# Kernel tuning notes

Hardware: AMD Instinct MI355X
Metric: run time of the kernel (lower is better)

## Reference

```python
import jax, jax.numpy as jnp
import numpy as np
import math

HIDDEN = 768
N_HEADS = 12
HEAD = HIDDEN // N_HEADS


def setup_inputs() -> dict:
    key = jax.random.key(0)
    k1, k2, k3, k4, k5 = jax.random.split(key, 5)
    x = jax.random.normal(k1, (2, 2048, HIDDEN), dtype=jnp.float32)
    s = 1.0 / math.sqrt(HIDDEN)
    W_qkv = jax.random.uniform(k2, (HIDDEN, 3 * HIDDEN), minval=-s, maxval=s, dtype=jnp.float32)
    b_qkv = jax.random.uniform(k3, (3 * HIDDEN,), minval=-s, maxval=s, dtype=jnp.float32)
    W_out = jax.random.uniform(k4, (HIDDEN, HIDDEN), minval=-s, maxval=s, dtype=jnp.float32)
    b_out = jax.random.uniform(k5, (HIDDEN,), minval=-s, maxval=s, dtype=jnp.float32)
    return {"x": x, "W_qkv": W_qkv, "b_qkv": b_qkv, "W_out": W_out, "b_out": b_out}


def reference(x, W_qkv, b_qkv, W_out, b_out):
    b, n, _ = x.shape
    qkv = x @ W_qkv + b_qkv                      # [b, n, 3H]
    q, k, v = jnp.split(qkv, 3, axis=-1)
    def heads(t):
        return t.reshape(b, n, N_HEADS, HEAD).transpose(0, 2, 1, 3)  # b h n l
    q, k, v = heads(q), heads(k), heads(v)
    scores = jnp.einsum('bhql,bhkl->bhqk', q, k) / math.sqrt(HEAD)
    mask = jnp.arange(n)[:, None] < jnp.arange(n)[None, :]  # True above diagonal
    scores = jnp.where(mask, jnp.float32(-10000.0), scores)
    attn = jax.nn.softmax(scores, axis=-1)
    out = jnp.einsum('bhqk,bhkl->bhql', attn, v)
    out = out.transpose(0, 2, 1, 3).reshape(b, n, HIDDEN)
    return out @ W_out + b_out
```

## Files before the change

kernel.cpp:

```cpp
#include <hip/hip_runtime.h>

typedef __attribute__((ext_vector_type(8))) short short8;
typedef __attribute__((ext_vector_type(4))) short short4v;
typedef __attribute__((ext_vector_type(4))) float floatx4;
typedef __attribute__((ext_vector_type(16))) float floatx16;

#define HIDDEN 768
#define NH 12
#define HD 64
#define SEQ 2048
#define BATCH 2
#define BHN (BATCH*NH)
#define MTOT (BATCH*SEQ)
#define NQKV (3*HIDDEN)
#define QSCALE 0.1803368801111204f

__device__ __forceinline__ short f2bf(float f) {
  union { float f; unsigned u; } v; v.f = f;
  unsigned r = v.u + 0x7FFFu + ((v.u >> 16) & 1u);
  return (short)(r >> 16);
}
__device__ __forceinline__ unsigned bfrne(float f) {
  unsigned u = __float_as_uint(f);
  return u + 0x7FFFu + ((u >> 16) & 1u);
}
__device__ __forceinline__ unsigned pk2(float a, float b) {
  return __builtin_amdgcn_perm(bfrne(b), bfrne(a), 0x07060302u);
}
__device__ __forceinline__ float bf2f(short s) {
  return __uint_as_float(((unsigned)(unsigned short)s) << 16);
}
__device__ __forceinline__ floatx4 mfma_bf16(short8 a, short8 b, floatx4 c) {
  return __builtin_amdgcn_mfma_f32_16x16x32_bf16(a, b, c, 0, 0, 0);
}
__device__ __forceinline__ floatx16 mfma32(short8 a, short8 b, floatx16 c) {
  return __builtin_amdgcn_mfma_f32_32x32x16_bf16(a, b, c, 0, 0, 0);
}
__device__ __forceinline__ short8 ld8(const short* p) {
  return *reinterpret_cast<const short8*>(p);
}
__device__ __forceinline__ void glds16(const short* g, short* l) {
  __builtin_amdgcn_global_load_lds(
      (const __attribute__((address_space(1))) void*)g,
      (__attribute__((address_space(3))) void*)l, 16, 0, 0);
}

__global__ __launch_bounds__(256) void prep(const float* __restrict__ X,
                                            const float* __restrict__ Wqkv,
                                            const float* __restrict__ Wout,
                                            short* __restrict__ Xb,
                                            short* __restrict__ WqkvT,
                                            short* __restrict__ WoutT) {
  __shared__ short t[64][72];
  int bx = blockIdx.x;
  if (bx < 1536) {
    int i = (bx * 256 + threadIdx.x) * 8;
    const float4* s = reinterpret_cast<const float4*>(X + i);
    float4 v0 = s[0], v1 = s[1];
    short8 o;
    o[0] = f2bf(v0.x); o[1] = f2bf(v0.y); o[2] = f2bf(v0.z); o[3] = f2bf(v0.w);
    o[4] = f2bf(v1.x); o[5] = f2bf(v1.y); o[6] = f2bf(v1.z); o[7] = f2bf(v1.w);
    *reinterpret_cast<short8*>(Xb + i) = o;
    return;
  }
  int tt = bx - 1536;
  int bxx = tt % 48, by = tt / 48;
  const float* W; short* WT; int N; int nb;
  if (bxx < 36) { W = Wqkv; WT = WqkvT; N = NQKV;   nb = bxx * 64; }
  else          { W = Wout; WT = WoutT; N = HIDDEN; nb = (bxx - 36) * 64; }
  int kb = by * 64;
  int tid = threadIdx.x;
  {
    int k  = tid >> 2;
    int n0 = (tid & 3) << 4;
    const float4* src = reinterpret_cast<const float4*>(W + (size_t)(kb + k) * N + nb + n0);
    #pragma unroll
    for (int c = 0; c < 4; ++c) {
      float4 v = src[c];
      t[n0 + c*4 + 0][k] = f2bf(v.x);
      t[n0 + c*4 + 1][k] = f2bf(v.y);
      t[n0 + c*4 + 2][k] = f2bf(v.z);
      t[n0 + c*4 + 3][k] = f2bf(v.w);
    }
  }
  __syncthreads();
  {
    int n  = tid >> 2;
    int k0 = (tid & 3) << 4;
    const short8* row = reinterpret_cast<const short8*>(&t[n][k0]);
    short8* dst = reinterpret_cast<short8*>(WT + (size_t)(nb + n) * HIDDEN + kb + k0);
    dst[0] = row[0];
    dst[1] = row[1];
  }
}

__global__ __launch_bounds__(256) void gemm_qkv(const short* __restrict__ Xb,
                                                const short* __restrict__ WT,
                                                const float* __restrict__ bias,
                                                short* __restrict__ Qb,
                                                short* __restrict__ Kb,
                                                short* __restrict__ VTb) {
  __shared__ short As[128 * 32];
  __shared__ short Bs[128 * 32];
  int m0 = blockIdx.x * 128, n0 = blockIdx.y * 128;
  int tid = threadIdx.x;
  int lane = tid & 63, wv = tid >> 6;
  int wm = (wv >> 1) << 6, wn = (wv & 1) << 6;
  int quad = lane >> 4, l16 = lane & 15;

  int srow = lane >> 2;
  int schunk = (lane & 3) ^ ((lane >> 3) & 3);
  const short* ag0 = Xb + (size_t)(m0 + wv * 32 + srow) * HIDDEN + schunk * 8;
  const short* ag1 = ag0 + 16 * HIDDEN;
  const short* bg0 = WT + (size_t)(n0 + wv * 32 + srow) * HIDDEN + schunk * 8;
  const short* bg1 = bg0 + 16 * HIDDEN;
  short* lA0 = As + wv * 1024;
  short* lB0 = Bs + wv * 1024;

  int sw = ((l16 >> 1) & 3);
  int aoff = (wm + l16) * 32 + ((quad ^ sw) << 3);
  int boff = (wn + l16) * 32 + ((quad ^ sw) << 3);

  floatx4 acc[4][4] = {};
  for (int kk = 0; kk < HIDDEN; kk += 32) {
    __syncthreads();
    glds16(ag0, lA0);
    glds16(ag1, lA0 + 512);
    glds16(bg0, lB0);
    glds16(bg1, lB0 + 512);
    ag0 += 32; ag1 += 32; bg0 += 32; bg1 += 32;
    __syncthreads();
    short8 af[4], bfr[4];
    #pragma unroll
    for (int i = 0; i < 4; ++i)
      af[i] = *reinterpret_cast<const short8*>(&As[aoff + i * 512]);
    #pragma unroll
    for (int j = 0; j < 4; ++j)
      bfr[j] = *reinterpret_cast<const short8*>(&Bs[boff + j * 512]);
    #pragma unroll
    for (int i = 0; i < 4; ++i)
      #pragma unroll
      for (int j = 0; j < 4; ++j)
        acc[i][j] = mfma_bf16(af[i], bfr[j], acc[i][j]);
  }
  int colbase = n0 + wn;
  int part = colbase / HIDDEN;
  #pragma unroll
  for (int j = 0; j < 4; ++j) {
    int col = colbase + j * 16 + l16;
    float bs = bias[col];
    int rem = col - part * HIDDEN;
    int h = rem >> 6, d = rem & 63;
    #pragma unroll
    for (int i = 0; i < 4; ++i) {
      #pragma unroll
      for (int r = 0; r < 4; ++r) {
        int row = m0 + wm + i * 16 + quad * 4 + r;
        float v = acc[i][j][r] + bs;
        int bb = row >> 11, s = row & 2047;
        int bh = bb * NH + h;
        if (part == 0) {
          Qb[((size_t)bh * SEQ + s) * HD + d] = f2bf(v * QSCALE);
        } else if (part == 1) {
          Kb[((size_t)bh * SEQ + s) * HD + d] = f2bf(v);
        } else {
          VTb[((size_t)bh * HD + d) * SEQ + s] = f2bf(v);
        }
      }
    }
  }
}

__global__ __launch_bounds__(256, 4) void attn_partial(const short* __restrict__ Qb,
                                                       const short* __restrict__ Kb,
                                                       const short* __restrict__ VTb,
                                                       short* __restrict__ PO,
                                                       float* __restrict__ PM,
                                                       float* __restrict__ PL) {
  __shared__ __align__(16) char lds[32768];
  int blk = blockIdx.x;
  int cls = blk & 7;
  int j   = blk >> 3;
  int headsel = j / 40;
  int bh  = cls + 8 * headsel;
  int cidx = 39 - (j - headsel * 40);
  int qt, c;
  if (cidx < 4)       { qt = cidx;                  c = 0; }
  else if (cidx < 12) { qt = 4 + ((cidx - 4) >> 1); c = (cidx - 4) & 1; }
  else if (cidx < 24) { int t = cidx - 12; int q3 = t / 3; qt = 8 + q3; c = t - 3 * q3; }
  else                { int t = cidx - 24; qt = 12 + (t >> 2); c = t & 3; }
  int g = qt >> 2, p = qt & 3;
  int idx = bh * 40 + (g + 1) * (2 * g + p) + c;

  int nt  = 2 * qt + 2;
  int kt0 = c * 8;
  int kt1 = min(nt, kt0 + 8);
  int qb0 = qt * 128;

  int tid = threadIdx.x;
  int lane = tid & 63, wv = tid >> 6;
  int l31 = lane & 31, h = lane >> 5, x = lane & 7;
  const short* Qp = Qb + (size_t)bh * SEQ * HD;
  const short* Kp = Kb + (size_t)bh * SEQ * HD;
  const short* Vp = VTb + (size_t)bh * HD * SEQ;

  int qs  = qb0 + wv * 32 + l31;
  int qlo = qb0 + wv * 32;
  int qhi = qlo + 31;

  short8 bq[4];
  #pragma unroll
  for (int dc = 0; dc < 4; ++dc)
    bq[dc] = ld8(Qp + qs * HD + dc * 16 + h * 8);

  int lr = lane >> 3;
  int cgc = (lane & 7) ^ lr;
  const short* kgl = Kp + (size_t)(kt0 * 64 + wv * 16 + lr) * HD + cgc * 8;
  const short* vgl = Vp + (size_t)(wv * 16 + lr) * SEQ + kt0 * 64 + cgc * 8;
  int wofs = wv * 2048;

  int rbase[4];
  #pragma unroll
  for (int kc = 0; kc < 4; ++kc)
    rbase[kc] = (l31 << 7) | ((((kc << 1) | h) ^ x) << 4);

  glds16(kgl,            (short*)(lds + wofs));
  glds16(kgl + 8 * HD,   (short*)(lds + wofs + 1024));
  glds16(vgl,            (short*)(lds + 16384 + wofs));
  glds16(vgl + 8 * SEQ,  (short*)(lds + 16384 + wofs + 1024));
  __syncthreads();

  floatx16 o0 = {}, o1 = {};
  float m_run = -1e30f, l_run = 0.f;

  for (int kt = kt0; kt < kt1; ++kt) {
    int cur = (kt - kt0) & 1;
    int curK = cur * 8192, curV = 16384 + cur * 8192;
    int kb = kt * 64;

    if (kt + 1 < kt1) {
      kgl += 64 * HD; vgl += 64;
      int nK = (cur ^ 1) * 8192, nV = 16384 + (cur ^ 1) * 8192;
      glds16(kgl,           (short*)(lds + nK + wofs));
      glds16(kgl + 8 * HD,  (short*)(lds + nK + wofs + 1024));
      glds16(vgl,           (short*)(lds + nV + wofs));
      glds16(vgl + 8 * SEQ, (short*)(lds + nV + wofs + 1024));
    }

    if (kb <= qhi) {
      floatx16 s0 = {}, s1 = {};
      #pragma unroll
      for (int kc = 0; kc < 4; ++kc) {
        short8 ka0 = *reinterpret_cast<const short8*>(lds + curK + rbase[kc]);
        short8 ka1 = *reinterpret_cast<const short8*>(lds + curK + 4096 + rbase[kc]);
        s0 = mfma32(ka0, bq[kc], s0);
        s1 = mfma32(ka1, bq[kc], s1);
      }
      if (kb + 63 > qlo) {
        #pragma unroll
        for (int r = 0; r < 16; ++r) {
          int kvr = kb + (r & 3) + 8 * (r >> 2) + 4 * h;
          s0[r] = (kvr > qs) ? -1e30f : s0[r];
          s1[r] = (kvr + 32 > qs) ? -1e30f : s1[r];
        }
      }
      float mloc = m_run;
      #pragma unroll
      for (int r = 0; r < 16; ++r) { mloc = fmaxf(mloc, s0[r]); mloc = fmaxf(mloc, s1[r]); }
      mloc = fmaxf(mloc, __shfl_xor(mloc, 32));
      float m_new = mloc;
      float alpha = __builtin_amdgcn_exp2f(m_run - m_new);
      float sloc = 0.f;
      #pragma unroll
      for (int r = 0; r < 16; ++r) {
        s0[r] = __builtin_amdgcn_exp2f(s0[r] - m_new); sloc += s0[r];
        s1[r] = __builtin_amdgcn_exp2f(s1[r] - m_new); sloc += s1[r];
      }
      sloc += __shfl_xor(sloc, 32);
      l_run = l_run * alpha + sloc;
      m_run = m_new;
      o0 *= alpha; o1 *= alpha;
      short8 pb[4];
      #pragma unroll
      for (int kvc = 0; kvc < 4; ++kvc) {
        int base = (kvc & 1) * 8;
        const floatx16& P = (kvc < 2) ? s0 : s1;
        unsigned e0 = pk2(P[base + 0], P[base + 1]);
        unsigned e1 = pk2(P[base + 2], P[base + 3]);
        unsigned f0 = pk2(P[base + 4], P[base + 5]);
        unsigned f1 = pk2(P[base + 6], P[base + 7]);
        unsigned k_0 = h ? f0 : e0, k_1 = h ? f1 : e1;
        unsigned s_0 = h ? e0 : f0, s_1 = h ? e1 : f1;
        unsigned r_0 = __shfl_xor((int)s_0, 32);
        unsigned r_1 = __shfl_xor((int)s_1, 32);
        union { unsigned u[4]; short8 v; } pbu;
        pbu.u[0] = h ? r_0 : k_0;
        pbu.u[1] = h ? r_1 : k_1;
        pbu.u[2] = h ? k_0 : r_0;
        pbu.u[3] = h ? k_1 : r_1;
        pb[kvc] = pbu.v;
      }
      #pragma unroll
      for (int kvc = 0; kvc < 4; ++kvc) {
        short8 va0 = *reinterpret_cast<const short8*>(lds + curV + rbase[kvc]);
        short8 va1 = *reinterpret_cast<const short8*>(lds + curV + 4096 + rbase[kvc]);
        o0 = mfma32(va0, pb[kvc], o0);
        o1 = mfma32(va1, pb[kvc], o1);
      }
    }
    __syncthreads();
  }

  int qloc = wv * 32 + l31;
  size_t pobase = (size_t)idx * 8192 + qloc * 64;
  #pragma unroll
  for (int dt = 0; dt < 2; ++dt) {
    #pragma unroll
    for (int cc = 0; cc < 4; ++cc) {
      int d = dt * 32 + 8 * cc + 4 * h;
      short4v w;
      #pragma unroll
      for (int r = 0; r < 4; ++r)
        w[r] = f2bf(dt ? o1[4 * cc + r] : o0[4 * cc + r]);
      *reinterpret_cast<short4v*>(PO + pobase + d) = w;
    }
  }
  if (h == 0) {
    PM[idx * 128 + qloc] = m_run;
    PL[idx * 128 + qloc] = l_run;
  }
}

__global__ __launch_bounds__(256) void attn_merge(const short* __restrict__ PO,
                                                  const float* __restrict__ PM,
                                                  const float* __restrict__ PL,
                                                  short* __restrict__ AO) {
  int blk = blockIdx.x;
  int bh = blk >> 4, qt = blk & 15;
  int g = qt >> 2, p = qt & 3;
  int base = bh * 40 + (g + 1) * (2 * g + p);
  int nc = g + 1;
  int tid = threadIdx.x;
  int q = tid >> 1, dh = (tid & 1) << 5;
  float mv[4];
  float M = -1e30f;
  for (int c = 0; c < nc; ++c) {
    mv[c] = PM[(base + c) * 128 + q];
    M = fmaxf(M, mv[c]);
  }
  float wsum = 0.f;
  float acc[32] = {};
  for (int c = 0; c < nc; ++c) {
    float w = __builtin_amdgcn_exp2f(mv[c] - M);
    wsum += PL[(base + c) * 128 + q] * w;
    const short8* po = reinterpret_cast<const short8*>(PO + (size_t)(base + c) * 8192 + q * 64 + dh);
    #pragma unroll
    for (int k = 0; k < 4; ++k) {
      short8 v = po[k];
      #pragma unroll
      for (int e = 0; e < 8; ++e)
        acc[k * 8 + e] += w * bf2f(v[e]);
    }
  }
  float inv = 1.f / wsum;
  int b = bh / NH, hh = bh % NH;
  int s = qt * 128 + q;
  short* dst = AO + ((size_t)(b * SEQ + s)) * HIDDEN + hh * HD + dh;
  #pragma unroll
  for (int k = 0; k < 4; ++k) {
    short8 w8;
    #pragma unroll
    for (int e = 0; e < 8; ++e)
      w8[e] = f2bf(acc[k * 8 + e] * inv);
    *reinterpret_cast<short8*>(dst + k * 8) = w8;
  }
}

__global__ __launch_bounds__(256) void gemm_out(const short* __restrict__ AO,
                                                const short* __restrict__ WT,
                                                const float* __restrict__ bias,
                                                float* __restrict__ out) {
  __shared__ short As[64 * 32];
  __shared__ short Bs[128 * 32];
  int m0 = blockIdx.x * 64, n0 = blockIdx.y * 128;
  int tid = threadIdx.x;
  int lane = tid & 63, wv = tid >> 6;
  int wm = (wv >> 1) << 5;
  int wn = (wv & 1) << 6;
  int quad = lane >> 4, l16 = lane & 15;

  int srow = lane >> 2;
  int schunk = (lane & 3) ^ ((lane >> 3) & 3);
  const short* ag  = AO + (size_t)(m0 + wv * 16 + srow) * HIDDEN + schunk * 8;
  const short* bg0 = WT + (size_t)(n0 + wv * 32 + srow) * HIDDEN + schunk * 8;
  const short* bg1 = bg0 + 16 * HIDDEN;
  short* lA  = As + wv * 512;
  short* lB0 = Bs + wv * 1024;

  int sw = ((l16 >> 1) & 3);
  int aoff = (wm + l16) * 32 + ((quad ^ sw) << 3);
  int boff = (wn + l16) * 32 + ((quad ^ sw) << 3);

  floatx4 acc[2][4] = {};
  for (int kk = 0; kk < HIDDEN; kk += 32) {
    __syncthreads();
    glds16(ag, lA);
    glds16(bg0, lB0);
    glds16(bg1, lB0 + 512);
    ag += 32; bg0 += 32; bg1 += 32;
    __syncthreads();
    short8 af[2], bfr[4];
    #pragma unroll
    for (int i = 0; i < 2; ++i)
      af[i] = *reinterpret_cast<const short8*>(&As[aoff + i * 512]);
    #pragma unroll
    for (int j = 0; j < 4; ++j)
      bfr[j] = *reinterpret_cast<const short8*>(&Bs[boff + j * 512]);
    #pragma unroll
    for (int i = 0; i < 2; ++i)
      #pragma unroll
      for (int j = 0; j < 4; ++j)
        acc[i][j] = mfma_bf16(af[i], bfr[j], acc[i][j]);
  }
  #pragma unroll
  for (int j = 0; j < 4; ++j) {
    int col = n0 + wn + j * 16 + l16;
    float bs = bias[col];
    #pragma unroll
    for (int i = 0; i < 2; ++i) {
      #pragma unroll
      for (int r = 0; r < 4; ++r) {
        int row = m0 + wm + i * 16 + quad * 4 + r;
        out[(size_t)row * HIDDEN + col] = acc[i][j][r] + bs;
      }
    }
  }
}

extern "C" void kernel_launch(void* const* d_in, const int* in_sizes, int n_in,
                              void* d_out, int out_size, void* d_ws, size_t ws_size,
                              hipStream_t stream) {
  const float* x    = (const float*)d_in[0];
  const float* Wqkv = (const float*)d_in[1];
  const float* bqkv = (const float*)d_in[2];
  const float* Wout = (const float*)d_in[3];
  const float* bout = (const float*)d_in[4];
  float* out = (float*)d_out;

  short* WqkvT = (short*)d_ws;
  short* WoutT = WqkvT + (size_t)NQKV * HIDDEN;
  short* Qb    = WoutT + (size_t)HIDDEN * HIDDEN;
  short* Kb    = Qb + (size_t)BHN * SEQ * HD;
  short* VTb   = Kb + (size_t)BHN * SEQ * HD;
  short* AO    = VTb + (size_t)BHN * SEQ * HD;
  short* Xb    = AO + (size_t)MTOT * HIDDEN;
  short* PO    = Xb;
  float* PM    = (float*)(PO + (size_t)960 * 8192);
  float* PL    = PM + 960 * 128;

  prep<<<dim3(2112), 256, 0, stream>>>(x, Wqkv, Wout, Xb, WqkvT, WoutT);
  gemm_qkv<<<dim3(MTOT / 128, NQKV / 128), 256, 0, stream>>>(Xb, WqkvT, bqkv, Qb, Kb, VTb);
  attn_partial<<<dim3(960), 256, 0, stream>>>(Qb, Kb, VTb, PO, PM, PL);
  attn_merge<<<dim3(BHN * 16), 256, 0, stream>>>(PO, PM, PL, AO);
  gemm_out<<<dim3(MTOT / 64, HIDDEN / 128), 256, 0, stream>>>(AO, WoutT, bout, out);
}
```

Measured before the change: 157.2 us.

## Fuse split-KV attention merge into output projection GEMM prologue

Removes the separate attn_merge kernel and AO buffer. The out-projection GEMM now computes per-row merge weights from PM/PL into shared memory, then builds each A tile on the fly by combining the partial outputs PO with those weights. This saves one launch and a write and re-read of AO. In exchange, the merge work is repeated across the 6 column blocks, and the A loads become synchronous vector loads with fp32 math inside the K loop instead of async global-to-LDS copies.

```diff
diff --git a/kernel.cpp b/kernel.cpp
--- a/kernel.cpp
+++ b/kernel.cpp
@@ -331,70 +331,55 @@
   }
 }
 
-__global__ __launch_bounds__(256) void attn_merge(const short* __restrict__ PO,
-                                                  const float* __restrict__ PM,
-                                                  const float* __restrict__ PL,
-                                                  short* __restrict__ AO) {
-  int blk = blockIdx.x;
-  int bh = blk >> 4, qt = blk & 15;
-  int g = qt >> 2, p = qt & 3;
-  int base = bh * 40 + (g + 1) * (2 * g + p);
-  int nc = g + 1;
-  int tid = threadIdx.x;
-  int q = tid >> 1, dh = (tid & 1) << 5;
-  float mv[4];
-  float M = -1e30f;
-  for (int c = 0; c < nc; ++c) {
-    mv[c] = PM[(base + c) * 128 + q];
-    M = fmaxf(M, mv[c]);
-  }
-  float wsum = 0.f;
-  float acc[32] = {};
-  for (int c = 0; c < nc; ++c) {
-    float w = __builtin_amdgcn_exp2f(mv[c] - M);
-    wsum += PL[(base + c) * 128 + q] * w;
-    const short8* po = reinterpret_cast<const short8*>(PO + (size_t)(base + c) * 8192 + q * 64 + dh);
-    #pragma unroll
-    for (int k = 0; k < 4; ++k) {
-      short8 v = po[k];
-      #pragma unroll
-      for (int e = 0; e < 8; ++e)
-        acc[k * 8 + e] += w * bf2f(v[e]);
-    }
-  }
-  float inv = 1.f / wsum;
-  int b = bh / NH, hh = bh % NH;
-  int s = qt * 128 + q;
-  short* dst = AO + ((size_t)(b * SEQ + s)) * HIDDEN + hh * HD + dh;
-  #pragma unroll
-  for (int k = 0; k < 4; ++k) {
-    short8 w8;
-    #pragma unroll
-    for (int e = 0; e < 8; ++e)
-      w8[e] = f2bf(acc[k * 8 + e] * inv);
-    *reinterpret_cast<short8*>(dst + k * 8) = w8;
-  }
-}
-
-__global__ __launch_bounds__(256) void gemm_out(const short* __restrict__ AO,
-                                                const short* __restrict__ WT,
-                                                const float* __restrict__ bias,
-                                                float* __restrict__ out) {
+__global__ __launch_bounds__(256) void gemm_out_fused(const short* __restrict__ PO,
+                                                      const float* __restrict__ PM,
+                                                      const float* __restrict__ PL,
+                                                      const short* __restrict__ WT,
+                                                      const float* __restrict__ bias,
+                                                      float* __restrict__ out) {
   __shared__ short As[64 * 32];
   __shared__ short Bs[128 * 32];
+  __shared__ float Wts[12][64][4];
   int m0 = blockIdx.x * 64, n0 = blockIdx.y * 128;
+  int b  = m0 >> 11;
+  int s0 = m0 & 2047;
+  int qt = s0 >> 7;
+  int g = qt >> 2, p = qt & 3;
+  int nc = g + 1;
+  int off = (g + 1) * (2 * g + p);
   int tid = threadIdx.x;
+
+  for (int pp = tid; pp < 768; pp += 256) {
+    int row = pp & 63, hh = pp >> 6;
+    int qloc = (s0 + row) & 127;
+    int ib = (b * NH + hh) * 40 + off;
+    float m[4], l[4], M = -1e30f;
+    for (int c = 0; c < nc; ++c) {
+      m[c] = PM[(ib + c) * 128 + qloc];
+      l[c] = PL[(ib + c) * 128 + qloc];
+      M = fmaxf(M, m[c]);
+    }
+    float wsum = 0.f, w[4];
+    for (int c = 0; c < nc; ++c) { w[c] = __builtin_amdgcn_exp2f(m[c] - M); wsum += l[c] * w[c]; }
+    float inv = 1.f / wsum;
+    for (int c = 0; c < nc; ++c) Wts[hh][row][c] = w[c] * inv;
+  }
+
   int lane = tid & 63, wv = tid >> 6;
   int wm = (wv >> 1) << 5;
   int wn = (wv & 1) << 6;
   int quad = lane >> 4, l16 = lane & 15;
 
+  int lr = lane >> 2, cc = lane & 3;
+  int row_in_blk = wv * 16 + lr;
+  int qloc_a = (s0 + row_in_blk) & 127;
+  short* awr = As + row_in_blk * 32 + ((cc ^ ((lr >> 1) & 3)) << 3);
+  size_t pbase = (size_t)(b * NH * 40 + off) * 8192 + qloc_a * 64 + cc * 8;
+
   int srow = lane >> 2;
   int schunk = (lane & 3) ^ ((lane >> 3) & 3);
-  const short* ag  = AO + (size_t)(m0 + wv * 16 + srow) * HIDDEN + schunk * 8;
   const short* bg0 = WT + (size_t)(n0 + wv * 32 + srow) * HIDDEN + schunk * 8;
   const short* bg1 = bg0 + 16 * HIDDEN;
-  short* lA  = As + wv * 512;
   short* lB0 = Bs + wv * 1024;
 
   int sw = ((l16 >> 1) & 3);
@@ -404,10 +389,25 @@
   floatx4 acc[2][4] = {};
   for (int kk = 0; kk < HIDDEN; kk += 32) {
     __syncthreads();
-    glds16(ag, lA);
     glds16(bg0, lB0);
     glds16(bg1, lB0 + 512);
-    ag += 32; bg0 += 32; bg1 += 32;
+    bg0 += 32; bg1 += 32;
+    {
+      int hh = kk >> 6, dh0 = kk & 63;
+      const short* pp0 = PO + (size_t)hh * 40 * 8192 + pbase + dh0;
+      const float* wr = Wts[hh][row_in_blk];
+      float a[8] = {};
+      for (int c = 0; c < nc; ++c) {
+        short8 v = ld8(pp0 + c * 8192);
+        float wc = wr[c];
+        #pragma unroll
+        for (int e = 0; e < 8; ++e) a[e] += wc * bf2f(v[e]);
+      }
+      short8 av;
+      #pragma unroll
+      for (int e = 0; e < 8; ++e) av[e] = f2bf(a[e]);
+      *reinterpret_cast<short8*>(awr) = av;
+    }
     __syncthreads();
     short8 af[2], bfr[4];
     #pragma unroll
@@ -461,6 +461,5 @@
   prep<<<dim3(2112), 256, 0, stream>>>(x, Wqkv, Wout, Xb, WqkvT, WoutT);
   gemm_qkv<<<dim3(MTOT / 128, NQKV / 128), 256, 0, stream>>>(Xb, WqkvT, bqkv, Qb, Kb, VTb);
   attn_partial<<<dim3(960), 256, 0, stream>>>(Qb, Kb, VTb, PO, PM, PL);
-  attn_merge<<<dim3(BHN * 16), 256, 0, stream>>>(PO, PM, PL, AO);
-  gemm_out<<<dim3(MTOT / 64, HIDDEN / 128), 256, 0, stream>>>(AO, WoutT, bout, out);
-}
+  gemm_out_fused<<<dim3(MTOT / 64, HIDDEN / 128), 256, 0, stream>>>(PO, PM, PL, WoutT, bout, out);
+}
```

Result: slower. 172.1 us (+9.5%).
